# Optimization experiments

Measured on AMD Instinct MI355X. Metric: run time of the kernel, lower is better.

Reference implementation:

```python
import jax, jax.numpy as jnp
import numpy as np

EPS_LA = 1e-8
BN_EPS = 1e-5


def setup_inputs() -> dict:
    N, IN_C, HID, OUT_C = 8192, 64, 64, 32
    key = jax.random.key(0)
    ks = jax.random.split(key, 8)
    X = jax.random.normal(ks[0], (N, IN_C), dtype=jnp.float32)
    La = jax.random.uniform(ks[1], (N,), dtype=jnp.float32)  # eigenvalues in [0,1)
    U = jax.random.normal(ks[2], (N, N), dtype=jnp.float32)  # eigenvector matrix
    # learnable params
    ve = jnp.array([7.0], dtype=jnp.float32)   # Velocity(7)
    ve2 = jnp.array([0.0], dtype=jnp.float32)  # Velocity(0)
    W_w = jax.random.normal(ks[3], (HID, IN_C), dtype=jnp.float32) / np.sqrt(IN_C)
    W_b = jnp.zeros((HID,), dtype=jnp.float32)
    bn_gamma = jnp.ones((HID,), dtype=jnp.float32)
    bn_beta = jnp.zeros((HID,), dtype=jnp.float32)
    mlp_w = jax.random.normal(ks[4], (OUT_C, HID), dtype=jnp.float32) / np.sqrt(HID)
    mlp_b = jnp.zeros((OUT_C,), dtype=jnp.float32)
    return {"X": X, "La": La, "U": U, "ve": ve, "ve2": ve2,
            "W_w": W_w, "W_b": W_b, "bn_gamma": bn_gamma, "bn_beta": bn_beta,
            "mlp_w": mlp_w, "mlp_b": mlp_b}


def reference(X, La, U, ve, ve2, W_w, W_b, bn_gamma, bn_beta, mlp_w, mlp_b):
    # Spectral filter eigenvalue scalings (Velocity modules: elementwise pow)
    V_La = jnp.power(La, ve[0])                                # [N]
    V_La2 = jnp.power((2.0 * (La - EPS_LA) - 1.0) ** 2 + 1.0, ve2[0])  # [N]
    # U @ diag(V) @ U^T @ X done as elementwise scaling in the spectral domain
    # (same math as the dense diag-matmul chain, O(N^2 d) instead of O(N^3))
    out = U @ (V_La[:, None] * (U.T @ X))    # [N, in_c]
    out = U @ (V_La2[:, None] * (U.T @ out)) # [N, in_c]
    # Linear W
    out = out @ W_w.T + W_b                  # [N, hid]
    hidden_emd = out
    # BatchNorm1d (training-mode batch statistics, biased variance)
    mean = jnp.mean(out, axis=0)
    var = jnp.mean((out - mean) ** 2, axis=0)
    out = (out - mean) * jax.lax.rsqrt(var + BN_EPS) * bn_gamma + bn_beta
    # ReLU; dropout is identity in deterministic/eval reference
    out = jax.nn.relu(out)
    out = out @ mlp_w.T + mlp_b              # [N, out_c]
    return (jax.nn.log_softmax(out, axis=1), hidden_emd)
```

## Files before the change

### kernel.cpp

```cpp
#include <hip/hip_runtime.h>
#include <hip/hip_bf16.h>

typedef __attribute__((ext_vector_type(4))) float f32x4;
typedef __attribute__((ext_vector_type(8))) short bf16x8;
typedef __attribute__((ext_vector_type(8))) unsigned short u16x8;

#define NN 8192
#define SK 8
#define KSL (NN / SK)
#define NT (KSL / 64)

__device__ __forceinline__ unsigned short f2bf(float f) {
    unsigned int u = __float_as_uint(f);
    u += 0x7fffu + ((u >> 16) & 1u);
    return (unsigned short)(u >> 16);
}

__device__ __forceinline__ void gload16(const float* g, float* l) {
    __builtin_amdgcn_global_load_lds(
        (const __attribute__((address_space(1))) unsigned int*)g,
        (__attribute__((address_space(3))) unsigned int*)l, 16, 0, 0);
}

__global__ __launch_bounds__(256) void prep_v(const float* __restrict__ La,
        const float* __restrict__ ve, const float* __restrict__ ve2,
        float* __restrict__ V1, float* __restrict__ V2) {
    int i = blockIdx.x * 256 + threadIdx.x;
    float la = La[i];
    V1[i] = powf(la, ve[0]);
    float b = 2.0f * (la - 1e-8f) - 1.0f;
    V2[i] = powf(b * b + 1.0f, ve2[0]);
}

template<int TM>
__global__ __launch_bounds__(256, 4) void spec_pass(const float* __restrict__ U,
        const unsigned short* __restrict__ FB, float* __restrict__ Pout) {
    __shared__ float tile[2][4096];
    const int tid = threadIdx.x;
    const int w = tid >> 6, l = tid & 63;
    const int lm = l & 15, g = l >> 4;
    const int x0 = blockIdx.x * 64;
    const int kbase = blockIdx.y * KSL;
    const int kb0 = kbase >> 5;
    const unsigned short* fbL = FB + (size_t)l * 8;

    f32x4 acc[4];
#pragma unroll
    for (int f = 0; f < 4; ++f) acc[f] = (f32x4)0.f;

#define STAGE(B, CT)                                                           \
    do {                                                                       \
        _Pragma("unroll")                                                      \
        for (int q_ = 0; q_ < 4; ++q_) {                                       \
            const int cc_ = 4 * w + q_;                                        \
            const int row_ = 4 * cc_ + (l >> 4);                               \
            const int su_ = (l & 15) ^ (row_ & 7);                             \
            const float* gp_ = U +                                             \
                (size_t)(TM ? (kbase + (CT) * 64 + row_) : (x0 + row_)) * NN + \
                (TM ? x0 : (kbase + (CT) * 64)) + su_ * 4;                     \
            gload16(gp_, &tile[B][cc_ * 256]);                                 \
        }                                                                      \
    } while (0)

#define LOADFB(R, CT)                                                          \
    do {                                                                       \
        _Pragma("unroll")                                                      \
        for (int sp_ = 0; sp_ < 2; ++sp_)                                      \
            _Pragma("unroll")                                                  \
            for (int f_ = 0; f_ < 4; ++f_)                                     \
                R[sp_][f_] = *(const bf16x8*)(fbL +                            \
                    ((size_t)((kb0 + 2 * (CT) + sp_) * 4 + f_)) * 512);        \
    } while (0)

#define COMPUTE(B, FBR)                                                        \
    do {                                                                       \
        _Pragma("unroll")                                                      \
        for (int sp_ = 0; sp_ < 2; ++sp_) {                                    \
            if (!TM) {                                                         \
                const float* rp_ = &tile[B][(16 * w + lm) * 64];               \
                const int m7_ = lm & 7;                                        \
                f32x4 p0_ = *(const f32x4*)(rp_ +                              \
                    (((8 * sp_ + 2 * g) ^ m7_) << 2));                         \
                f32x4 p1_ = *(const f32x4*)(rp_ +                              \
                    (((8 * sp_ + 2 * g + 1) ^ m7_) << 2));                     \
                bf16x8 afr_;                                                   \
                _Pragma("unroll")                                              \
                for (int j_ = 0; j_ < 4; ++j_) {                               \
                    afr_[j_]     = (short)f2bf(p0_[j_]);                       \
                    afr_[4 + j_] = (short)f2bf(p1_[j_]);                       \
                }                                                              \
                _Pragma("unroll")                                              \
                for (int f_ = 0; f_ < 4; ++f_)                                 \
                    acc[f_] = __builtin_amdgcn_mfma_f32_16x16x32_bf16(         \
                        afr_, FBR[sp_][f_], acc[f_], 0, 0, 0);                 \
            } else {                                                           \
                bf16x8 bfr_;                                                   \
                _Pragma("unroll")                                              \
                for (int s_ = 0; s_ < 8; ++s_)                                 \
                    bfr_[s_] = (short)f2bf(tile[B][                            \
                        (32 * sp_ + 8 * g + s_) * 64 +                         \
                        (((4 * w + (lm >> 2)) ^ s_) << 2) + (lm & 3)]);        \
                _Pragma("unroll")                                              \
                for (int f_ = 0; f_ < 4; ++f_)                                 \
                    acc[f_] = __builtin_amdgcn_mfma_f32_16x16x32_bf16(         \
                        FBR[sp_][f_], bfr_, acc[f_], 0, 0, 0);                 \
            }                                                                  \
        }                                                                      \
    } while (0)

    bf16x8 fbA[2][4], fbB[2][4];
    LOADFB(fbA, 0);
    STAGE(0, 0);
    __syncthreads();
#pragma unroll 1
    for (int c = 0; c < NT; c += 2) {
        if (c + 1 < NT) { LOADFB(fbB, c + 1); STAGE(1, c + 1); }
        COMPUTE(0, fbA);
        __syncthreads();
        if (c + 2 < NT) { LOADFB(fbA, c + 2); STAGE(0, c + 2); }
        COMPUTE(1, fbB);
        __syncthreads();
    }
#undef STAGE
#undef LOADFB
#undef COMPUTE

    if (!TM) {
        float* Pp = Pout + (size_t)blockIdx.y * NN * 64;
#pragma unroll
        for (int f = 0; f < 4; ++f)
#pragma unroll
            for (int r = 0; r < 4; ++r)
                Pp[(size_t)(x0 + 16 * w + 4 * g + r) * 64 + f * 16 + lm] = acc[f][r];
    } else {
        float* Pp = Pout + (size_t)blockIdx.y * 64 * NN;
#pragma unroll
        for (int f = 0; f < 4; ++f)
#pragma unroll
            for (int r = 0; r < 4; ++r)
                Pp[(size_t)(16 * f + 4 * g + r) * NN + x0 + 16 * w + lm] = acc[f][r];
    }
}

__global__ __launch_bounds__(256) void reduce2(const float* __restrict__ Pt,
        const float* __restrict__ V, unsigned short* __restrict__ FB) {
    int b = blockIdx.x;
    int t = threadIdx.x;
    int nf = t >> 6, l = t & 63, lm = l & 15, g = l >> 4;
    int ch = 16 * nf + lm;
    int ib = 32 * b + 8 * g;
    f32x4 s0 = (f32x4)0.f, s1 = (f32x4)0.f;
#pragma unroll
    for (int sk = 0; sk < SK; ++sk) {
        const float* p = Pt + (size_t)(sk * 64 + ch) * NN + ib;
        s0 += *(const f32x4*)p;
        s1 += *(const f32x4*)(p + 4);
    }
    f32x4 v0 = *(const f32x4*)(V + ib);
    f32x4 v1 = *(const f32x4*)(V + ib + 4);
    u16x8 o;
#pragma unroll
    for (int c = 0; c < 4; ++c) {
        o[c]     = f2bf(s0[c] * v0[c]);
        o[4 + c] = f2bf(s1[c] * v1[c]);
    }
    *(u16x8*)(FB + ((size_t)(b * 4 + nf) * 64 + l) * 8) = o;
}

__global__ __launch_bounds__(256) void reduce_t(const float* __restrict__ M, int nsk,
        unsigned short* __restrict__ FB) {
    __shared__ float T[32][65];
    int b = blockIdx.x;
    int i0 = b * 32;
    int tid = threadIdx.x;
    int il = tid >> 3, jq = (tid & 7) * 8;
    f32x4 s0 = (f32x4)0.f, s1 = (f32x4)0.f;
    for (int k = 0; k < nsk; ++k) {
        const float* p = M + ((size_t)k * NN + i0 + il) * 64 + jq;
        s0 += *(const f32x4*)p;
        s1 += *(const f32x4*)(p + 4);
    }
#pragma unroll
    for (int c = 0; c < 4; ++c) {
        T[il][jq + c] = s0[c];
        T[il][jq + 4 + c] = s1[c];
    }
    __syncthreads();
    int nf = tid >> 6, l = tid & 63, g = l >> 4, lm = l & 15;
    u16x8 o;
#pragma unroll
    for (int s = 0; s < 8; ++s) o[s] = f2bf(T[8 * g + s][16 * nf + lm]);
    *(u16x8*)(FB + ((size_t)(b * 4 + nf) * 64 + l) * 8) = o;
}

__global__ __launch_bounds__(256) void reduce_linear(const float* __restrict__ P,
        const float* __restrict__ Ww, const float* __restrict__ Wb,
        float* __restrict__ hidden, float* __restrict__ bsum, float* __restrict__ bsq) {
    __shared__ float z[32][65];
    __shared__ float w[64][65];
    __shared__ float hl[32][65];
    int i0 = blockIdx.x * 32;
    int tid = threadIdx.x;
    for (int e = tid * 4; e < 4096; e += 1024) {
        f32x4 v = *(const f32x4*)(Ww + e);
        int h = e >> 6, c = e & 63;
#pragma unroll
        for (int q = 0; q < 4; ++q) w[h][c + q] = v[q];
    }
    int r = tid >> 3, c8 = (tid & 7) * 8;
    f32x4 a0 = (f32x4)0.f, a1 = (f32x4)0.f;
    for (int k = 0; k < SK; ++k) {
        const float* p = P + ((size_t)k * NN + i0 + r) * 64 + c8;
        a0 += *(const f32x4*)p;
        a1 += *(const f32x4*)(p + 4);
    }
#pragma unroll
    for (int q = 0; q < 4; ++q) { z[r][c8 + q] = a0[q]; z[r][c8 + 4 + q] = a1[q]; }
    __syncthreads();
    int h8 = (tid & 7) * 8;
#pragma unroll
    for (int hh = 0; hh < 8; ++hh) {
        int h = h8 + hh;
        float s = Wb[h];
        for (int c = 0; c < 64; ++c) s += z[r][c] * w[h][c];
        hidden[(size_t)(i0 + r) * 64 + h] = s;
        hl[r][h] = s;
    }
    __syncthreads();
    if (tid < 64) {
        float s = 0.f, q2 = 0.f;
#pragma unroll
        for (int rr = 0; rr < 32; ++rr) {
            float v = hl[rr][tid];
            s += v; q2 += v * v;
        }
        bsum[blockIdx.x * 64 + tid] = s;
        bsq[blockIdx.x * 64 + tid] = q2;
    }
}

__global__ __launch_bounds__(64) void bn_stats(const float* __restrict__ bsum,
        const float* __restrict__ bsq, const float* __restrict__ gamma,
        const float* __restrict__ beta, float* __restrict__ bnc) {
    int h = threadIdx.x;
    float s = 0.f, q = 0.f;
    for (int b = 0; b < 256; ++b) { s += bsum[b * 64 + h]; q += bsq[b * 64 + h]; }
    float mean = s / 8192.0f;
    float var = q / 8192.0f - mean * mean;
    float inv = rsqrtf(var + 1e-5f);
    float sc = gamma[h] * inv;
    bnc[h] = sc;
    bnc[64 + h] = beta[h] - mean * sc;
}

__global__ __launch_bounds__(256) void head(const float* __restrict__ hidden,
        const float* __restrict__ bnc, const float* __restrict__ Mw,
        const float* __restrict__ Mb, float* __restrict__ out0) {
    __shared__ float a[32][65];
    __shared__ float w[32][65];
    __shared__ float o[32][33];
    __shared__ float rowm[32];
    int i0 = blockIdx.x * 32;
    int tid = threadIdx.x;
    for (int e = tid * 4; e < 2048; e += 1024) {
        f32x4 v = *(const f32x4*)(Mw + e);
        int oo = e >> 6, c = e & 63;
#pragma unroll
        for (int q = 0; q < 4; ++q) w[oo][c + q] = v[q];
    }
    int r = tid >> 3, h8 = (tid & 7) * 8;
    const float* hp = hidden + (size_t)(i0 + r) * 64 + h8;
#pragma unroll
    for (int q = 0; q < 8; ++q) {
        int h = h8 + q;
        float v = hp[q] * bnc[h] + bnc[64 + h];
        a[r][h] = fmaxf(v, 0.f);
    }
    __syncthreads();
    int o4 = (tid & 7) * 4;
#pragma unroll
    for (int q = 0; q < 4; ++q) {
        int oo = o4 + q;
        float s = Mb[oo];
        for (int c = 0; c < 64; ++c) s += a[r][c] * w[oo][c];
        o[r][oo] = s;
    }
    __syncthreads();
    if (tid < 32) {
        float m = -3.0e38f;
#pragma unroll
        for (int c = 0; c < 32; ++c) m = fmaxf(m, o[tid][c]);
        float se = 0.f;
#pragma unroll
        for (int c = 0; c < 32; ++c) se += expf(o[tid][c] - m);
        rowm[tid] = m + logf(se);
    }
    __syncthreads();
    f32x4 v;
#pragma unroll
    for (int q = 0; q < 4; ++q) v[q] = o[r][o4 + q] - rowm[r];
    *(f32x4*)(out0 + (size_t)(i0 + r) * 32 + o4) = v;
}

extern "C" void kernel_launch(void* const* d_in, const int* in_sizes, int n_in,
                              void* d_out, int out_size, void* d_ws, size_t ws_size,
                              hipStream_t stream) {
    const float* X   = (const float*)d_in[0];
    const float* La  = (const float*)d_in[1];
    const float* U   = (const float*)d_in[2];
    const float* ve  = (const float*)d_in[3];
    const float* ve2 = (const float*)d_in[4];
    const float* Ww  = (const float*)d_in[5];
    const float* Wb  = (const float*)d_in[6];
    const float* gam = (const float*)d_in[7];
    const float* bet = (const float*)d_in[8];
    const float* Mw  = (const float*)d_in[9];
    const float* Mb  = (const float*)d_in[10];
    float* out0 = (float*)d_out;
    float* hidden = (float*)d_out + (size_t)NN * 32;

    char* ws = (char*)d_ws;
    float* V1   = (float*)ws;
    float* V2   = (float*)(ws + 32768);
    float* bsum = (float*)(ws + 65536);
    float* bsq  = (float*)(ws + 131072);
    float* bnc  = (float*)(ws + 196608);
    unsigned short* FB = (unsigned short*)(ws + 262144);
    float* P    = (float*)(ws + (2u << 20));
    float* Pt   = (float*)(ws + (20u << 20));

    prep_v<<<32, 256, 0, stream>>>(La, ve, ve2, V1, V2);
    reduce_t<<<256, 256, 0, stream>>>(X, 1, FB);
    spec_pass<1><<<dim3(NN / 64, SK), 256, 0, stream>>>(U, FB, Pt);
    reduce2<<<256, 256, 0, stream>>>(Pt, V1, FB);
    spec_pass<0><<<dim3(NN / 64, SK), 256, 0, stream>>>(U, FB, P);
    reduce_t<<<256, 256, 0, stream>>>(P, SK, FB);
    spec_pass<1><<<dim3(NN / 64, SK), 256, 0, stream>>>(U, FB, Pt);
    reduce2<<<256, 256, 0, stream>>>(Pt, V2, FB);
    spec_pass<0><<<dim3(NN / 64, SK), 256, 0, stream>>>(U, FB, P);
    reduce_linear<<<256, 256, 0, stream>>>(P, Ww, Wb, hidden, bsum, bsq);
    bn_stats<<<1, 64, 0, stream>>>(bsum, bsq, gam, bet, bnc);
    head<<<256, 256, 0, stream>>>(hidden, bnc, Mw, Mb, out0);
}
```

Before: 252.0 us.

## Emit a bf16 copy of U in the first pass and reuse it later

The first spectral pass still reads U in fp32, but it now also writes the converted bf16 tile back to a workspace copy of U. The other three passes read that bf16 copy through new LDS layouts and fragment loads, so they skip the per-element fp32-to-bf16 conversion. Each later pass reads half as many bytes of U. In exchange, the first pass pays an extra 128MB write and needs a large workspace region.

```diff
diff --git a/kernel.cpp b/kernel.cpp
--- a/kernel.cpp
+++ b/kernel.cpp
@@ -4,6 +4,7 @@
 typedef __attribute__((ext_vector_type(4))) float f32x4;
 typedef __attribute__((ext_vector_type(8))) short bf16x8;
 typedef __attribute__((ext_vector_type(8))) unsigned short u16x8;
+typedef __attribute__((ext_vector_type(4))) unsigned short u16x4;
 
 #define NN 8192
 #define SK 8
@@ -16,7 +17,7 @@
     return (unsigned short)(u >> 16);
 }
 
-__device__ __forceinline__ void gload16(const float* g, float* l) {
+__device__ __forceinline__ void gload16(const void* g, void* l) {
     __builtin_amdgcn_global_load_lds(
         (const __attribute__((address_space(1))) unsigned int*)g,
         (__attribute__((address_space(3))) unsigned int*)l, 16, 0, 0);
@@ -32,9 +33,10 @@
     V2[i] = powf(b * b + 1.0f, ve2[0]);
 }
 
-template<int TM>
-__global__ __launch_bounds__(256, 4) void spec_pass(const float* __restrict__ U,
-        const unsigned short* __restrict__ FB, float* __restrict__ Pout) {
+template<int TM, int BF, int EMIT>
+__global__ __launch_bounds__(256, 4) void spec_pass(const void* __restrict__ Usrc,
+        const unsigned short* __restrict__ FB, float* __restrict__ Pout,
+        unsigned short* __restrict__ Uemit) {
     __shared__ float tile[2][4096];
     const int tid = threadIdx.x;
     const int w = tid >> 6, l = tid & 63;
@@ -50,15 +52,30 @@
 
 #define STAGE(B, CT)                                                           \
     do {                                                                       \
-        _Pragma("unroll")                                                      \
-        for (int q_ = 0; q_ < 4; ++q_) {                                       \
-            const int cc_ = 4 * w + q_;                                        \
-            const int row_ = 4 * cc_ + (l >> 4);                               \
-            const int su_ = (l & 15) ^ (row_ & 7);                             \
-            const float* gp_ = U +                                             \
-                (size_t)(TM ? (kbase + (CT) * 64 + row_) : (x0 + row_)) * NN + \
-                (TM ? x0 : (kbase + (CT) * 64)) + su_ * 4;                     \
-            gload16(gp_, &tile[B][cc_ * 256]);                                 \
+        if (!BF) {                                                             \
+            _Pragma("unroll")                                                  \
+            for (int q_ = 0; q_ < 4; ++q_) {                                   \
+                const int cc_ = 4 * w + q_;                                    \
+                const int row_ = 4 * cc_ + (l >> 4);                           \
+                const int su_ = (l & 15) ^ (row_ & 7);                         \
+                const float* gp_ = (const float*)Usrc +                        \
+                    (size_t)(TM ? (kbase + (CT) * 64 + row_) : (x0 + row_))    \
+                        * NN +                                                 \
+                    (TM ? x0 : (kbase + (CT) * 64)) + su_ * 4;                 \
+                gload16(gp_, &tile[B][cc_ * 256]);                             \
+            }                                                                  \
+        } else {                                                               \
+            _Pragma("unroll")                                                  \
+            for (int q_ = 0; q_ < 2; ++q_) {                                   \
+                const int cc_ = 2 * w + q_;                                    \
+                const int row_ = 8 * cc_ + (l >> 3);                           \
+                const int su_ = (l & 7) ^ (row_ & 7);                          \
+                const unsigned short* gp_ = (const unsigned short*)Usrc +      \
+                    (size_t)(TM ? (kbase + (CT) * 64 + row_) : (x0 + row_))    \
+                        * NN +                                                 \
+                    (TM ? x0 : (kbase + (CT) * 64)) + su_ * 8;                 \
+                gload16(gp_, (unsigned short*)&tile[B][0] + cc_ * 512);        \
+            }                                                                  \
         }                                                                      \
     } while (0)
 
@@ -77,17 +94,25 @@
         _Pragma("unroll")                                                      \
         for (int sp_ = 0; sp_ < 2; ++sp_) {                                    \
             if (!TM) {                                                         \
-                const float* rp_ = &tile[B][(16 * w + lm) * 64];               \
-                const int m7_ = lm & 7;                                        \
-                f32x4 p0_ = *(const f32x4*)(rp_ +                              \
-                    (((8 * sp_ + 2 * g) ^ m7_) << 2));                         \
-                f32x4 p1_ = *(const f32x4*)(rp_ +                              \
-                    (((8 * sp_ + 2 * g + 1) ^ m7_) << 2));                     \
                 bf16x8 afr_;                                                   \
-                _Pragma("unroll")                                              \
-                for (int j_ = 0; j_ < 4; ++j_) {                               \
-                    afr_[j_]     = (short)f2bf(p0_[j_]);                       \
-                    afr_[4 + j_] = (short)f2bf(p1_[j_]);                       \
+                if (!BF) {                                                     \
+                    const float* rp_ = &tile[B][(16 * w + lm) * 64];           \
+                    const int m7_ = lm & 7;                                    \
+                    f32x4 p0_ = *(const f32x4*)(rp_ +                          \
+                        (((8 * sp_ + 2 * g) ^ m7_) << 2));                     \
+                    f32x4 p1_ = *(const f32x4*)(rp_ +                          \
+                        (((8 * sp_ + 2 * g + 1) ^ m7_) << 2));                 \
+                    _Pragma("unroll")                                          \
+                    for (int j_ = 0; j_ < 4; ++j_) {                           \
+                        afr_[j_]     = (short)f2bf(p0_[j_]);                   \
+                        afr_[4 + j_] = (short)f2bf(p1_[j_]);                   \
+                    }                                                          \
+                } else {                                                       \
+                    const unsigned short* rp_ =                                \
+                        (const unsigned short*)&tile[B][0] +                   \
+                        (16 * w + lm) * 64;                                    \
+                    afr_ = *(const bf16x8*)(rp_ +                              \
+                        (((4 * sp_ + g) ^ (lm & 7)) << 3));                    \
                 }                                                              \
                 _Pragma("unroll")                                              \
                 for (int f_ = 0; f_ < 4; ++f_)                                 \
@@ -95,11 +120,23 @@
                         afr_, FBR[sp_][f_], acc[f_], 0, 0, 0);                 \
             } else {                                                           \
                 bf16x8 bfr_;                                                   \
-                _Pragma("unroll")                                              \
-                for (int s_ = 0; s_ < 8; ++s_)                                 \
-                    bfr_[s_] = (short)f2bf(tile[B][                            \
-                        (32 * sp_ + 8 * g + s_) * 64 +                         \
-                        (((4 * w + (lm >> 2)) ^ s_) << 2) + (lm & 3)]);        \
+                if (!BF) {                                                     \
+                    _Pragma("unroll")                                          \
+                    for (int s_ = 0; s_ < 8; ++s_)                             \
+                        bfr_[s_] = (short)f2bf(tile[B][                        \
+                            (32 * sp_ + 8 * g + s_) * 64 +                     \
+                            (((4 * w + (lm >> 2)) ^ s_) << 2) + (lm & 3)]);    \
+                } else {                                                       \
+                    const unsigned short* t16_ =                               \
+                        (const unsigned short*)&tile[B][0];                    \
+                    _Pragma("unroll")                                          \
+                    for (int s_ = 0; s_ < 8; ++s_) {                           \
+                        const int k_ = 32 * sp_ + 8 * g + s_;                  \
+                        bfr_[s_] = (short)t16_[k_ * 64 +                       \
+                            (((2 * w + (lm >> 3)) ^ (k_ & 7)) << 3) +          \
+                            (lm & 7)];                                         \
+                    }                                                          \
+                }                                                              \
                 _Pragma("unroll")                                              \
                 for (int f_ = 0; f_ < 4; ++f_)                                 \
                     acc[f_] = __builtin_amdgcn_mfma_f32_16x16x32_bf16(         \
@@ -108,6 +145,25 @@
         }                                                                      \
     } while (0)
 
+#define ECHO(B, CT)                                                            \
+    do {                                                                       \
+        if (EMIT) {                                                            \
+            _Pragma("unroll")                                                  \
+            for (int q_ = 0; q_ < 4; ++q_) {                                   \
+                const int cc_ = 4 * w + q_;                                    \
+                const int row_ = 4 * cc_ + (l >> 4);                           \
+                const int su_ = (l & 15) ^ (row_ & 7);                         \
+                f32x4 v_ = *(const f32x4*)&tile[B][cc_ * 256 + l * 4];         \
+                u16x4 h_;                                                      \
+                _Pragma("unroll")                                              \
+                for (int q2_ = 0; q2_ < 4; ++q2_) h_[q2_] = f2bf(v_[q2_]);     \
+                *(u16x4*)(Uemit +                                              \
+                    (size_t)(kbase + (CT) * 64 + row_) * NN + x0 + su_ * 4)    \
+                    = h_;                                                      \
+            }                                                                  \
+        }                                                                      \
+    } while (0)
+
     bf16x8 fbA[2][4], fbB[2][4];
     LOADFB(fbA, 0);
     STAGE(0, 0);
@@ -116,14 +172,17 @@
     for (int c = 0; c < NT; c += 2) {
         if (c + 1 < NT) { LOADFB(fbB, c + 1); STAGE(1, c + 1); }
         COMPUTE(0, fbA);
+        ECHO(0, c);
         __syncthreads();
         if (c + 2 < NT) { LOADFB(fbA, c + 2); STAGE(0, c + 2); }
         COMPUTE(1, fbB);
+        ECHO(1, c + 1);
         __syncthreads();
     }
 #undef STAGE
 #undef LOADFB
 #undef COMPUTE
+#undef ECHO
 
     if (!TM) {
         float* Pp = Pout + (size_t)blockIdx.y * NN * 64;
@@ -328,16 +387,17 @@
     unsigned short* FB = (unsigned short*)(ws + 262144);
     float* P    = (float*)(ws + (2u << 20));
     float* Pt   = (float*)(ws + (20u << 20));
+    unsigned short* Ubf = (unsigned short*)(ws + (64u << 20));
 
     prep_v<<<32, 256, 0, stream>>>(La, ve, ve2, V1, V2);
     reduce_t<<<256, 256, 0, stream>>>(X, 1, FB);
-    spec_pass<1><<<dim3(NN / 64, SK), 256, 0, stream>>>(U, FB, Pt);
+    spec_pass<1, 0, 1><<<dim3(NN / 64, SK), 256, 0, stream>>>(U, FB, Pt, Ubf);
     reduce2<<<256, 256, 0, stream>>>(Pt, V1, FB);
-    spec_pass<0><<<dim3(NN / 64, SK), 256, 0, stream>>>(U, FB, P);
+    spec_pass<0, 1, 0><<<dim3(NN / 64, SK), 256, 0, stream>>>(Ubf, FB, P, nullptr);
     reduce_t<<<256, 256, 0, stream>>>(P, SK, FB);
-    spec_pass<1><<<dim3(NN / 64, SK), 256, 0, stream>>>(U, FB, Pt);
+    spec_pass<1, 1, 0><<<dim3(NN / 64, SK), 256, 0, stream>>>(Ubf, FB, Pt, nullptr);
     reduce2<<<256, 256, 0, stream>>>(Pt, V2, FB);
-    spec_pass<0><<<dim3(NN / 64, SK), 256, 0, stream>>>(U, FB, P);
+    spec_pass<0, 1, 0><<<dim3(NN / 64, SK), 256, 0, stream>>>(Ubf, FB, P, nullptr);
     reduce_linear<<<256, 256, 0, stream>>>(P, Ww, Wb, hidden, bsum, bsq);
     bn_stats<<<1, 64, 0, stream>>>(bsum, bsq, gam, bet, bnc);
     head<<<256, 256, 0, stream>>>(hidden, bnc, Mw, Mb, out0);
```

New measurement: 277.9 us. +10.3%, slower.

## Emit bf16 copy of U in first pass and stream it in later passes

Applied to the files above, without the earlier changes.

The first spectral pass now writes a bf16 copy of U into workspace while it computes, reading the fp32 tile already staged in LDS. The remaining three passes run a new bf16-tile kernel that reads this half-size copy, which halves the HBM traffic for U in those passes. The cost is an extra 128MB write in the first pass and extra workspace. Precision is unchanged because the MFMA already consumed bf16-rounded U.

```diff
diff --git a/kernel.cpp b/kernel.cpp
--- a/kernel.cpp
+++ b/kernel.cpp
@@ -4,11 +4,13 @@
 typedef __attribute__((ext_vector_type(4))) float f32x4;
 typedef __attribute__((ext_vector_type(8))) short bf16x8;
 typedef __attribute__((ext_vector_type(8))) unsigned short u16x8;
+typedef __attribute__((ext_vector_type(4))) unsigned short u16x4;
 
 #define NN 8192
 #define SK 8
 #define KSL (NN / SK)
 #define NT (KSL / 64)
+#define NTB (KSL / 128)
 
 __device__ __forceinline__ unsigned short f2bf(float f) {
     unsigned int u = __float_as_uint(f);
@@ -16,7 +18,7 @@
     return (unsigned short)(u >> 16);
 }
 
-__device__ __forceinline__ void gload16(const float* g, float* l) {
+__device__ __forceinline__ void gload16(const void* g, void* l) {
     __builtin_amdgcn_global_load_lds(
         (const __attribute__((address_space(1))) unsigned int*)g,
         (__attribute__((address_space(3))) unsigned int*)l, 16, 0, 0);
@@ -32,9 +34,10 @@
     V2[i] = powf(b * b + 1.0f, ve2[0]);
 }
 
-template<int TM>
-__global__ __launch_bounds__(256, 4) void spec_pass(const float* __restrict__ U,
-        const unsigned short* __restrict__ FB, float* __restrict__ Pout) {
+template<int TM, int BF, int EMIT>
+__global__ __launch_bounds__(256, 4) void spec_pass(const void* __restrict__ Usrc,
+        const unsigned short* __restrict__ FB, float* __restrict__ Pout,
+        unsigned short* __restrict__ Uemit) {
     __shared__ float tile[2][4096];
     const int tid = threadIdx.x;
     const int w = tid >> 6, l = tid & 63;
@@ -55,7 +58,7 @@
             const int cc_ = 4 * w + q_;                                        \
             const int row_ = 4 * cc_ + (l >> 4);                               \
             const int su_ = (l & 15) ^ (row_ & 7);                             \
-            const float* gp_ = U +                                             \
+            const float* gp_ = (const float*)Usrc +                            \
                 (size_t)(TM ? (kbase + (CT) * 64 + row_) : (x0 + row_)) * NN + \
                 (TM ? x0 : (kbase + (CT) * 64)) + su_ * 4;                     \
             gload16(gp_, &tile[B][cc_ * 256]);                                 \
@@ -108,6 +111,25 @@
         }                                                                      \
     } while (0)
 
+#define ECHO(B, CT)                                                            \
+    do {                                                                       \
+        if (EMIT) {                                                            \
+            _Pragma("unroll")                                                  \
+            for (int q_ = 0; q_ < 4; ++q_) {                                   \
+                const int cc_ = 4 * w + q_;                                    \
+                const int row_ = 4 * cc_ + (l >> 4);                           \
+                const int su_ = (l & 15) ^ (row_ & 7);                         \
+                f32x4 v_ = *(const f32x4*)&tile[B][cc_ * 256 + l * 4];         \
+                u16x4 h_;                                                      \
+                _Pragma("unroll")                                              \
+                for (int q2_ = 0; q2_ < 4; ++q2_) h_[q2_] = f2bf(v_[q2_]);     \
+                *(u16x4*)(Uemit +                                              \
+                    (size_t)(kbase + (CT) * 64 + row_) * NN + x0 + su_ * 4)    \
+                    = h_;                                                      \
+            }                                                                  \
+        }                                                                      \
+    } while (0)
+
     bf16x8 fbA[2][4], fbB[2][4];
     LOADFB(fbA, 0);
     STAGE(0, 0);
@@ -116,14 +138,120 @@
     for (int c = 0; c < NT; c += 2) {
         if (c + 1 < NT) { LOADFB(fbB, c + 1); STAGE(1, c + 1); }
         COMPUTE(0, fbA);
+        ECHO(0, c);
         __syncthreads();
         if (c + 2 < NT) { LOADFB(fbA, c + 2); STAGE(0, c + 2); }
         COMPUTE(1, fbB);
+        ECHO(1, c + 1);
         __syncthreads();
     }
 #undef STAGE
 #undef LOADFB
 #undef COMPUTE
+#undef ECHO
+
+    if (!TM) {
+        float* Pp = Pout + (size_t)blockIdx.y * NN * 64;
+#pragma unroll
+        for (int f = 0; f < 4; ++f)
+#pragma unroll
+            for (int r = 0; r < 4; ++r)
+                Pp[(size_t)(x0 + 16 * w + 4 * g + r) * 64 + f * 16 + lm] = acc[f][r];
+    } else {
+        float* Pp = Pout + (size_t)blockIdx.y * 64 * NN;
+#pragma unroll
+        for (int f = 0; f < 4; ++f)
+#pragma unroll
+            for (int r = 0; r < 4; ++r)
+                Pp[(size_t)(16 * f + 4 * g + r) * NN + x0 + 16 * w + lm] = acc[f][r];
+    }
+}
+
+template<int TM>
+__global__ __launch_bounds__(256, 4) void spec_bf16(
+        const unsigned short* __restrict__ Ub,
+        const unsigned short* __restrict__ FB, float* __restrict__ Pout) {
+    __shared__ unsigned short tile[2][8192];
+    const int tid = threadIdx.x;
+    const int w = tid >> 6, l = tid & 63;
+    const int lm = l & 15, g = l >> 4;
+    const int x0 = blockIdx.x * 64;
+    const int kbase = blockIdx.y * KSL;
+    const int kb0 = kbase >> 5;
+    const unsigned short* fbL = FB + (size_t)l * 8;
+
+    f32x4 acc[4];
+#pragma unroll
+    for (int f = 0; f < 4; ++f) acc[f] = (f32x4)0.f;
+
+#define STG(B, CT)                                                             \
+    do {                                                                       \
+        _Pragma("unroll")                                                      \
+        for (int q_ = 0; q_ < 4; ++q_) {                                       \
+            const int cc_ = 4 * w + q_;                                        \
+            if (!TM) {                                                         \
+                const int row_ = 4 * cc_ + (l >> 4);                           \
+                const int su_ = lm ^ (row_ & 7);                               \
+                const unsigned short* gp_ = Ub +                               \
+                    (size_t)(x0 + row_) * NN + kbase + (CT) * 128 + su_ * 8;   \
+                gload16(gp_, &tile[B][cc_ * 512]);                             \
+            } else {                                                           \
+                const int row_ = 8 * cc_ + (l >> 3);                           \
+                const int su_ = (l & 7) ^ (row_ & 7);                          \
+                const unsigned short* gp_ = Ub +                               \
+                    (size_t)(kbase + (CT) * 128 + row_) * NN + x0 + su_ * 8;   \
+                gload16(gp_, &tile[B][cc_ * 512]);                             \
+            }                                                                  \
+        }                                                                      \
+    } while (0)
+
+#define CMP(B, CT)                                                             \
+    do {                                                                       \
+        _Pragma("unroll")                                                      \
+        for (int sp_ = 0; sp_ < 4; ++sp_) {                                    \
+            if (!TM) {                                                         \
+                const unsigned short* rp_ = &tile[B][(16 * w + lm) * 128];     \
+                bf16x8 afr_ = *(const bf16x8*)(rp_ +                           \
+                    (((4 * sp_ + g) ^ (lm & 7)) << 3));                        \
+                _Pragma("unroll")                                              \
+                for (int f_ = 0; f_ < 4; ++f_) {                               \
+                    bf16x8 bf_ = *(const bf16x8*)(fbL +                        \
+                        ((size_t)((kb0 + 4 * (CT) + sp_) * 4 + f_)) * 512);    \
+                    acc[f_] = __builtin_amdgcn_mfma_f32_16x16x32_bf16(         \
+                        afr_, bf_, acc[f_], 0, 0, 0);                          \
+                }                                                              \
+            } else {                                                           \
+                bf16x8 bfr_;                                                   \
+                _Pragma("unroll")                                              \
+                for (int s_ = 0; s_ < 8; ++s_) {                               \
+                    const int k_ = 32 * sp_ + 8 * g + s_;                      \
+                    bfr_[s_] = (short)tile[B][k_ * 64 +                        \
+                        (((2 * w + (lm >> 3)) ^ (k_ & 7)) << 3) + (lm & 7)];   \
+                }                                                              \
+                _Pragma("unroll")                                              \
+                for (int f_ = 0; f_ < 4; ++f_) {                               \
+                    bf16x8 af_ = *(const bf16x8*)(fbL +                        \
+                        ((size_t)((kb0 + 4 * (CT) + sp_) * 4 + f_)) * 512);    \
+                    acc[f_] = __builtin_amdgcn_mfma_f32_16x16x32_bf16(         \
+                        af_, bfr_, acc[f_], 0, 0, 0);                          \
+                }                                                              \
+            }                                                                  \
+        }                                                                      \
+    } while (0)
+
+    STG(0, 0);
+    __syncthreads();
+#pragma unroll 1
+    for (int c = 0; c < NTB; c += 2) {
+        if (c + 1 < NTB) STG(1, c + 1);
+        CMP(0, c);
+        __syncthreads();
+        if (c + 2 < NTB) STG(0, c + 2);
+        CMP(1, c + 1);
+        __syncthreads();
+    }
+#undef STG
+#undef CMP
 
     if (!TM) {
         float* Pp = Pout + (size_t)blockIdx.y * NN * 64;
@@ -328,16 +456,17 @@
     unsigned short* FB = (unsigned short*)(ws + 262144);
     float* P    = (float*)(ws + (2u << 20));
     float* Pt   = (float*)(ws + (20u << 20));
+    unsigned short* Ubf = (unsigned short*)(ws + (64u << 20));
 
     prep_v<<<32, 256, 0, stream>>>(La, ve, ve2, V1, V2);
     reduce_t<<<256, 256, 0, stream>>>(X, 1, FB);
-    spec_pass<1><<<dim3(NN / 64, SK), 256, 0, stream>>>(U, FB, Pt);
+    spec_pass<1, 0, 1><<<dim3(NN / 64, SK), 256, 0, stream>>>(U, FB, Pt, Ubf);
     reduce2<<<256, 256, 0, stream>>>(Pt, V1, FB);
-    spec_pass<0><<<dim3(NN / 64, SK), 256, 0, stream>>>(U, FB, P);
+    spec_bf16<0><<<dim3(NN / 64, SK), 256, 0, stream>>>(Ubf, FB, P);
     reduce_t<<<256, 256, 0, stream>>>(P, SK, FB);
-    spec_pass<1><<<dim3(NN / 64, SK), 256, 0, stream>>>(U, FB, Pt);
+    spec_bf16<1><<<dim3(NN / 64, SK), 256, 0, stream>>>(Ubf, FB, Pt);
     reduce2<<<256, 256, 0, stream>>>(Pt, V2, FB);
-    spec_pass<0><<<dim3(NN / 64, SK), 256, 0, stream>>>(U, FB, P);
+    spec_bf16<0><<<dim3(NN / 64, SK), 256, 0, stream>>>(Ubf, FB, P);
     reduce_linear<<<256, 256, 0, stream>>>(P, Ww, Wb, hidden, bsum, bsq);
     bn_stats<<<1, 64, 0, stream>>>(bsum, bsq, gam, bet, bnc);
     head<<<256, 256, 0, stream>>>(hidden, bnc, Mw, Mb, out0);
```

After: 278.8 us. 10.6% more time.
